# Kernel optimization log

Hardware: AMD Instinct MI355X
Metric: run time of the kernel (lower is better)

The kernel has to match this reference:

```python
import jax, jax.numpy as jnp
import numpy as np
from functools import partial

T, B, V, E, H = 512, 64, 256, 256, 512  # seq, batch, vocab, embed, lstm_hidden


def _lstm_dir(x_proj, W_hh, h0, c0):
    # x_proj: [T, B, 4H] (input projection + bias precomputed); scan only the recurrent matmul
    def step(carry, xp):
        h, c = carry
        gates = xp + h @ W_hh.T                       # [B, 4H]
        i, f, g, o = jnp.split(gates, 4, axis=-1)     # PyTorch gate order i,f,g,o
        i = jax.nn.sigmoid(i); f = jax.nn.sigmoid(f)
        g = jnp.tanh(g); o = jax.nn.sigmoid(o)
        c = f * c + i * g
        h = o * jnp.tanh(c)
        return (h, c), h
    _, hs = jax.lax.scan(step, (h0, c0), x_proj)
    return hs  # [T, B, H]


def setup_inputs() -> dict:
    key = jax.random.key(0)
    ks = jax.random.split(key, 10)
    u = lambda k, shape, s: jax.random.uniform(k, shape, jnp.float32, -s, s)
    bound = 1.0 / np.sqrt(H)
    return {
        "tokens": jax.random.randint(ks[0], (T, B), 0, V, dtype=jnp.int32),
        "h0": jnp.zeros((2, B, H), jnp.float32),
        "c0": jnp.zeros((2, B, H), jnp.float32),
        "embed_table": jax.random.normal(ks[1], (V, E), jnp.float32),
        "W_ih_f": u(ks[2], (4 * H, E), bound),
        "W_hh_f": u(ks[3], (4 * H, H), bound),
        "b_f": u(ks[4], (4 * H,), bound),   # b_ih + b_hh fused
        "W_ih_b": u(ks[5], (4 * H, E), bound),
        "W_hh_b": u(ks[6], (4 * H, H), bound),
        "b_b": u(ks[7], (4 * H,), bound),
        "W_W": u(ks[8], (2 * H, 2 * H), 0.1),
        "b_att": jnp.zeros((2 * H,), jnp.float32),  # bias_char [2H,1] squeezed; uninit in torch
        "w_proj": u(ks[9], (2 * H,), 0.1),           # weight_proj_char [2H,1] squeezed
    }


def reference(tokens, h0, c0, embed_table, W_ih_f, W_hh_f, b_f,
              W_ih_b, W_hh_b, b_b, W_W, b_att, w_proj):
    embedded = embed_table[tokens]                           # [T, B, E]
    # forward direction
    xp_f = jnp.einsum('tbe,ge->tbg', embedded, W_ih_f) + b_f
    out_f = _lstm_dir(xp_f, W_hh_f, h0[0], c0[0])            # [T, B, H]
    # backward direction (reverse time)
    xp_b = jnp.einsum('tbe,ge->tbg', embedded[::-1], W_ih_b) + b_b
    out_b = _lstm_dir(xp_b, W_hh_b, h0[1], c0[1])[::-1]      # [T, B, H]
    output = jnp.concatenate([out_f, out_b], axis=-1)        # [T, B, 2H]
    # additive attention: tanh(out @ W_W + b) . w_proj, softmax over T
    squish = jnp.tanh(jnp.einsum('tbh,hk->tbk', output, W_W) + b_att)
    scores = jnp.einsum('tbk,k->tb', squish, w_proj)         # [T, B]
    attn = jax.nn.softmax(scores, axis=0)                    # softmax over time
    char_vectors = jnp.einsum('tb,tbh->bh', attn, output)    # [B, 2H]
    return char_vectors
```

## Files before the change

kernel.cpp:

```cpp
#include <hip/hip_runtime.h>

#define T_   512
#define B_   64
#define V_   256
#define E_   256
#define H_   512
#define NWGD 32
#define THR  256

typedef _Float16 f16;
typedef _Float16 f16x8 __attribute__((ext_vector_type(8)));
typedef _Float16 f16x4 __attribute__((ext_vector_type(4)));
typedef float    f32x4 __attribute__((ext_vector_type(4)));

#define WS_CTL      0
#define WS_CTL_END  8192
#define WS_SCORES   WS_CTL_END
#define WS_ATTN     (WS_SCORES + 512*64*4)
#define WS_ZERO_END (WS_ATTN + 512*64*4)
#define WS_TAB      WS_ZERO_END
#define WS_WARR     (WS_TAB + 256*256*2)
#define WS_WWT      (WS_WARR + 2*2048*768*2)
#define WS_HBUF     (WS_WWT + 1024*1024*2)
#define WS_OUT      (WS_HBUF + 2*2*64*512*2)
#define WS_END      (WS_OUT + (size_t)512*64*1024*2)

__device__ inline int load_int_sc1(const int* p) {
    int v;
    asm volatile("global_load_dword %0, %1, off sc1\n\ts_waitcnt vmcnt(0)"
                 : "=v"(v) : "v"(p) : "memory");
    return v;
}

__device__ inline void store_int_sc1(int* p, int v) {
    asm volatile("global_store_dword %0, %1, off sc1"
                 :: "v"(p), "v"(v) : "memory");
}

__device__ inline void store_f16_sc1(f16* p, float x) {
    f16 h = (f16)x;
    unsigned int w = (unsigned int)__builtin_bit_cast(unsigned short, h);
    asm volatile("global_store_short %0, %1, off sc1"
                 :: "v"(p), "v"(w) : "memory");
}

__device__ inline void load8_sc1(const f16* p,
    f16x8& r0, f16x8& r1, f16x8& r2, f16x8& r3,
    f16x8& r4, f16x8& r5, f16x8& r6, f16x8& r7) {
    asm volatile(
        "global_load_dwordx4 %0, %8, off sc1\n\t"
        "global_load_dwordx4 %1, %8, off offset:16 sc1\n\t"
        "global_load_dwordx4 %2, %8, off offset:32 sc1\n\t"
        "global_load_dwordx4 %3, %8, off offset:48 sc1\n\t"
        "global_load_dwordx4 %4, %8, off offset:64 sc1\n\t"
        "global_load_dwordx4 %5, %8, off offset:80 sc1\n\t"
        "global_load_dwordx4 %6, %8, off offset:96 sc1\n\t"
        "global_load_dwordx4 %7, %8, off offset:112 sc1\n\t"
        "s_waitcnt vmcnt(0)"
        : "=&v"(r0), "=&v"(r1), "=&v"(r2), "=&v"(r3),
          "=&v"(r4), "=&v"(r5), "=&v"(r6), "=&v"(r7)
        : "v"(p) : "memory");
}

__device__ inline void drain_vm() {
    asm volatile("s_waitcnt vmcnt(0)" ::: "memory");
}

__global__ void k_setup_table(const float* __restrict__ et, f16* __restrict__ tab) {
    int i = blockIdx.x * 256 + threadIdx.x;
    tab[i] = (f16)et[i];
}

__global__ void k_setup_wwt(const float* __restrict__ ww, f16* __restrict__ wwt) {
    int i = blockIdx.x * 256 + threadIdx.x;
    int col = i >> 10, h = i & 1023;
    wwt[(col << 10) + h] = (f16)ww[(h << 10) + col];
}

__global__ void k_setup_warr(const float* __restrict__ wihf, const float* __restrict__ whhf,
                             const float* __restrict__ wihb, const float* __restrict__ whhb,
                             f16* __restrict__ warr) {
    int i = blockIdx.x * 256 + threadIdx.x;
    int k = i % 768;
    int r = i / 768;
    int colp = r & 63;
    int wg   = (r >> 6) & 31;
    int dir  = r >> 11;
    int gate = colp >> 4, u = colp & 15;
    int row = gate * 512 + wg * 16 + u;
    const float* wih = dir ? wihb : wihf;
    const float* whh = dir ? whhb : whhf;
    float v = (k < 256) ? wih[row * 256 + k] : whh[row * 512 + (k - 256)];
    warr[i] = (f16)v;
}

#define A_ROWB  1536
#define LDS_A_BYTES   (64 * A_ROWB)
#define LDS_G_BYTES   (64 * 65 * 4)
#define LDS_C_BYTES   (64 * 16 * 4)
#define LDS_TOTAL     (LDS_A_BYTES + LDS_G_BYTES + LDS_C_BYTES)

__device__ inline int swz(int row, int byteInRow) {
    return byteInRow ^ ((((byteInRow >> 8) + 5 * row) & 7) << 4);
}

__launch_bounds__(THR, 1)
__global__ void k_lstm(const int* __restrict__ tokens,
                       const float* __restrict__ h0, const float* __restrict__ c0,
                       const float* __restrict__ b_f, const float* __restrict__ b_b,
                       const f16* __restrict__ tab, const f16* __restrict__ warr,
                       f16* __restrict__ hbuf, f16* __restrict__ outcat,
                       int* __restrict__ ctl) {
    extern __shared__ __align__(16) char smem[];
    char*  A    = smem;
    float* gate = (float*)(smem + LDS_A_BYTES);
    float* cst  = (float*)(smem + LDS_A_BYTES + LDS_G_BYTES);

    const int tid = threadIdx.x;
    const int dir = blockIdx.x >> 5, wg = blockIdx.x & 31;

    int* flags = ctl + 64 + dir * 512;

    const int l = tid & 63, w = tid >> 6;
    const int mh = w >> 1, nh = w & 1;

    f16x8 bf[2][24];
#pragma unroll
    for (int n = 0; n < 2; ++n) {
#pragma unroll
        for (int kt = 0; kt < 24; ++kt) {
            int colp = nh * 32 + n * 16 + (l & 15);
            long off = ((long)((dir * 32 + wg) * 64 + colp)) * 768 + kt * 32 + (l >> 4) * 8;
            bf[n][kt] = *(const f16x8*)(warr + off);
        }
    }
    const float* bv = dir ? b_b : b_f;
    const int u_t = tid & 15;
    float bias[4];
#pragma unroll
    for (int g = 0; g < 4; ++g) bias[g] = bv[g * 512 + wg * 16 + u_t];

#pragma unroll
    for (int r = 0; r < 4; ++r) {
        int p = r * 256 + tid;
        int b = p >> 4, u = p & 15;
        int ug = wg * 16 + u;
        cst[b * 16 + u] = c0[(dir * 64 + b) * 512 + ug];
        store_f16_sc1(hbuf + ((0 * 2 + dir) * 64 + b) * 512 + ug,
                      h0[(dir * 64 + b) * 512 + ug]);
    }
    drain_vm();
    __syncthreads();
    if (tid == 0) store_int_sc1(flags + wg * 16, 1);

    const int row_t = tid >> 2, part = tid & 3;

#pragma unroll 1
    for (int s = 0; s < 512; ++s) {
        const int t_act = dir ? (511 - s) : s;

        {
            int tok = tokens[t_act * 64 + row_t];
            const f16* src = tab + tok * 256 + part * 64;
            char* base = A + row_t * A_ROWB;
            f16x8 e[8];
#pragma unroll
            for (int c = 0; c < 8; ++c) e[c] = *(const f16x8*)(src + c * 8);
#pragma unroll
            for (int c = 0; c < 8; ++c)
                *(f16x8*)(base + swz(row_t, part * 128 + c * 16)) = e[c];
        }

        {
            const int* fp = flags + (l & 31) * 16;
            const int target = s + 1;
            int guard = 0;
            while (true) {
                int v = load_int_sc1(fp);
                if (__all(v >= target)) break;
                if (++guard > 32768) break;
            }
        }

        {
            const f16* src = hbuf + (((s & 1) * 2 + dir) * 64 + row_t) * 512 + part * 128;
            char* base = A + row_t * A_ROWB;
            f16x8 r0, r1, r2, r3, r4, r5, r6, r7;
            load8_sc1(src, r0, r1, r2, r3, r4, r5, r6, r7);
            *(f16x8*)(base + swz(row_t, 512 + part * 256 +   0)) = r0;
            *(f16x8*)(base + swz(row_t, 512 + part * 256 +  16)) = r1;
            *(f16x8*)(base + swz(row_t, 512 + part * 256 +  32)) = r2;
            *(f16x8*)(base + swz(row_t, 512 + part * 256 +  48)) = r3;
            *(f16x8*)(base + swz(row_t, 512 + part * 256 +  64)) = r4;
            *(f16x8*)(base + swz(row_t, 512 + part * 256 +  80)) = r5;
            *(f16x8*)(base + swz(row_t, 512 + part * 256 +  96)) = r6;
            *(f16x8*)(base + swz(row_t, 512 + part * 256 + 112)) = r7;
            load8_sc1(src + 64, r0, r1, r2, r3, r4, r5, r6, r7);
            *(f16x8*)(base + swz(row_t, 512 + part * 256 + 128)) = r0;
            *(f16x8*)(base + swz(row_t, 512 + part * 256 + 144)) = r1;
            *(f16x8*)(base + swz(row_t, 512 + part * 256 + 160)) = r2;
            *(f16x8*)(base + swz(row_t, 512 + part * 256 + 176)) = r3;
            *(f16x8*)(base + swz(row_t, 512 + part * 256 + 192)) = r4;
            *(f16x8*)(base + swz(row_t, 512 + part * 256 + 208)) = r5;
            *(f16x8*)(base + swz(row_t, 512 + part * 256 + 224)) = r6;
            *(f16x8*)(base + swz(row_t, 512 + part * 256 + 240)) = r7;
        }
        __syncthreads();

        f32x4 acc[2][2];
#pragma unroll
        for (int m = 0; m < 2; ++m)
#pragma unroll
            for (int n = 0; n < 2; ++n)
                acc[m][n] = (f32x4){0.f, 0.f, 0.f, 0.f};
        const int arow0 = mh * 32 + (l & 15);
        const int koffB = (l >> 4) * 16;
#pragma unroll
        for (int kt = 0; kt < 24; ++kt) {
            int binr = kt * 64 + koffB;
            f16x8 a0 = *(const f16x8*)(A + arow0 * A_ROWB + swz(arow0, binr));
            f16x8 a1 = *(const f16x8*)(A + (arow0 + 16) * A_ROWB + swz(arow0 + 16, binr));
            acc[0][0] = __builtin_amdgcn_mfma_f32_16x16x32_f16(a0, bf[0][kt], acc[0][0], 0, 0, 0);
            acc[0][1] = __builtin_amdgcn_mfma_f32_16x16x32_f16(a0, bf[1][kt], acc[0][1], 0, 0, 0);
            acc[1][0] = __builtin_amdgcn_mfma_f32_16x16x32_f16(a1, bf[0][kt], acc[1][0], 0, 0, 0);
            acc[1][1] = __builtin_amdgcn_mfma_f32_16x16x32_f16(a1, bf[1][kt], acc[1][1], 0, 0, 0);
        }
#pragma unroll
        for (int m = 0; m < 2; ++m)
#pragma unroll
            for (int n = 0; n < 2; ++n)
#pragma unroll
                for (int q = 0; q < 4; ++q) {
                    int brow = mh * 32 + m * 16 + (l >> 4) * 4 + q;
                    int col  = nh * 32 + n * 16 + (l & 15);
                    gate[brow * 65 + col] = acc[m][n][q];
                }
        __syncthreads();

#pragma unroll
        for (int r = 0; r < 4; ++r) {
            int p = r * 256 + tid;
            int b = p >> 4, u = p & 15;
            float gi = gate[b * 65 +  0 + u] + bias[0];
            float gf = gate[b * 65 + 16 + u] + bias[1];
            float gg = gate[b * 65 + 32 + u] + bias[2];
            float go = gate[b * 65 + 48 + u] + bias[3];
            float si = 1.f / (1.f + __expf(-gi));
            float sf = 1.f / (1.f + __expf(-gf));
            float tg = tanhf(gg);
            float so = 1.f / (1.f + __expf(-go));
            float c = sf * cst[b * 16 + u] + si * tg;
            float h = so * tanhf(c);
            cst[b * 16 + u] = c;
            int ug = wg * 16 + u;
            store_f16_sc1(hbuf + ((((s + 1) & 1) * 2 + dir) * 64 + b) * 512 + ug, h);
            outcat[((long)t_act * 64 + b) * 1024 + dir * 512 + ug] = (f16)h;
        }
        drain_vm();
        __syncthreads();
        if (tid == 0) store_int_sc1(flags + wg * 16, s + 2);
    }
}

__global__ void k_attn_gemm(const f16* __restrict__ outcat, const f16* __restrict__ wwt,
                            const float* __restrict__ b_att, const float* __restrict__ w_proj,
                            float* __restrict__ scores) {
    __shared__ __align__(16) f16 A2[64][136];
    __shared__ __align__(16) f16 B2[64][136];
    __shared__ float sq[64][68];
    const int tid = threadIdx.x;
    const int mb = blockIdx.x >> 4, nb = blockIdx.x & 15;
    const int r0 = mb * 64, c0 = nb * 64;
    const int l = tid & 63, w = tid >> 6;
    const int mh = w >> 1, nhf = w & 1;

    f32x4 acc[2][2];
#pragma unroll
    for (int m = 0; m < 2; ++m)
#pragma unroll
        for (int n = 0; n < 2; ++n)
            acc[m][n] = (f32x4){0.f, 0.f, 0.f, 0.f};

    for (int kc = 0; kc < 8; ++kc) {
        int k0 = kc * 128;
        {
            int row = tid >> 2, seg = tid & 3;
            const f16* sa = outcat + (long)(r0 + row) * 1024 + k0 + seg * 32;
            const f16* sb = wwt + (long)(c0 + row) * 1024 + k0 + seg * 32;
#pragma unroll
            for (int j = 0; j < 4; ++j) {
                *(f16x8*)(&A2[row][seg * 32 + j * 8]) = *(const f16x8*)(sa + j * 8);
                *(f16x8*)(&B2[row][seg * 32 + j * 8]) = *(const f16x8*)(sb + j * 8);
            }
        }
        __syncthreads();
        const int kofs = (l >> 4) * 8;
#pragma unroll
        for (int kt = 0; kt < 4; ++kt) {
            int ko = kt * 32 + kofs;
            f16x8 a0 = *(const f16x8*)(&A2[mh * 32 + (l & 15)][ko]);
            f16x8 a1 = *(const f16x8*)(&A2[mh * 32 + 16 + (l & 15)][ko]);
            f16x8 b0 = *(const f16x8*)(&B2[nhf * 32 + (l & 15)][ko]);
            f16x8 b1 = *(const f16x8*)(&B2[nhf * 32 + 16 + (l & 15)][ko]);
            acc[0][0] = __builtin_amdgcn_mfma_f32_16x16x32_f16(a0, b0, acc[0][0], 0, 0, 0);
            acc[0][1] = __builtin_amdgcn_mfma_f32_16x16x32_f16(a0, b1, acc[0][1], 0, 0, 0);
            acc[1][0] = __builtin_amdgcn_mfma_f32_16x16x32_f16(a1, b0, acc[1][0], 0, 0, 0);
            acc[1][1] = __builtin_amdgcn_mfma_f32_16x16x32_f16(a1, b1, acc[1][1], 0, 0, 0);
        }
        __syncthreads();
    }
#pragma unroll
    for (int m = 0; m < 2; ++m)
#pragma unroll
        for (int n = 0; n < 2; ++n)
#pragma unroll
            for (int q = 0; q < 4; ++q) {
                int rl = mh * 32 + m * 16 + (l >> 4) * 4 + q;
                int cl = nhf * 32 + n * 16 + (l & 15);
                int cg = c0 + cl;
                sq[rl][cl] = tanhf(acc[m][n][q] + b_att[cg]) * w_proj[cg];
            }
    __syncthreads();
    if (tid < 64) {
        float s = 0.f;
#pragma unroll
        for (int c2 = 0; c2 < 64; ++c2) s += sq[tid][c2];
        atomicAdd(scores + r0 + tid, s);
    }
}

__global__ void k_softmax(const float* __restrict__ scores, float* __restrict__ attn) {
    const int b = blockIdx.x, tid = threadIdx.x;
    __shared__ float redm[4];
    __shared__ float reds[4];
    float v0 = scores[(tid * 2 + 0) * 64 + b];
    float v1 = scores[(tid * 2 + 1) * 64 + b];
    float m = fmaxf(v0, v1);
#pragma unroll
    for (int off = 32; off; off >>= 1) m = fmaxf(m, __shfl_down(m, off));
    if ((tid & 63) == 0) redm[tid >> 6] = m;
    __syncthreads();
    m = fmaxf(fmaxf(redm[0], redm[1]), fmaxf(redm[2], redm[3]));
    float e0 = __expf(v0 - m), e1 = __expf(v1 - m);
    float s = e0 + e1;
#pragma unroll
    for (int off = 32; off; off >>= 1) s += __shfl_down(s, off);
    if ((tid & 63) == 0) reds[tid >> 6] = s;
    __syncthreads();
    s = (reds[0] + reds[1]) + (reds[2] + reds[3]);
    float inv = 1.f / s;
    attn[(tid * 2 + 0) * 64 + b] = e0 * inv;
    attn[(tid * 2 + 1) * 64 + b] = e1 * inv;
}

__global__ void k_wsum(const float* __restrict__ attn, const f16* __restrict__ outcat,
                       float* __restrict__ out) {
    const int b = blockIdx.x, tid = threadIdx.x;
    float a0 = 0.f, a1 = 0.f, a2 = 0.f, a3 = 0.f;
    for (int t = 0; t < 512; ++t) {
        float at = attn[t * 64 + b];
        f16x4 v = *(const f16x4*)(outcat + ((long)t * 64 + b) * 1024 + tid * 4);
        a0 += at * (float)v[0];
        a1 += at * (float)v[1];
        a2 += at * (float)v[2];
        a3 += at * (float)v[3];
    }
    float* dst = out + b * 1024 + tid * 4;
    dst[0] = a0; dst[1] = a1; dst[2] = a2; dst[3] = a3;
}

extern "C" void kernel_launch(void* const* d_in, const int* in_sizes, int n_in,
                              void* d_out, int out_size, void* d_ws, size_t ws_size,
                              hipStream_t stream) {
    if (ws_size < WS_END) return;

    const int*   tokens = (const int*)d_in[0];
    const float* h0     = (const float*)d_in[1];
    const float* c0     = (const float*)d_in[2];
    const float* etab   = (const float*)d_in[3];
    const float* wihf   = (const float*)d_in[4];
    const float* whhf   = (const float*)d_in[5];
    const float* b_f    = (const float*)d_in[6];
    const float* wihb   = (const float*)d_in[7];
    const float* whhb   = (const float*)d_in[8];
    const float* b_b    = (const float*)d_in[9];
    const float* ww     = (const float*)d_in[10];
    const float* b_att  = (const float*)d_in[11];
    const float* w_proj = (const float*)d_in[12];
    float* out = (float*)d_out;

    char* ws = (char*)d_ws;
    int*   ctl    = (int*)(ws + WS_CTL);
    float* scores = (float*)(ws + WS_SCORES);
    float* attn   = (float*)(ws + WS_ATTN);
    f16*   tab    = (f16*)(ws + WS_TAB);
    f16*   warr   = (f16*)(ws + WS_WARR);
    f16*   wwt    = (f16*)(ws + WS_WWT);
    f16*   hbuf   = (f16*)(ws + WS_HBUF);
    f16*   outcat = (f16*)(ws + WS_OUT);

    hipMemsetAsync(d_ws, 0, WS_ZERO_END, stream);

    k_setup_table<<<256, 256, 0, stream>>>(etab, tab);
    k_setup_wwt<<<4096, 256, 0, stream>>>(ww, wwt);
    k_setup_warr<<<12288, 256, 0, stream>>>(wihf, whhf, wihb, whhb, warr);

    static int lds_set = 0;
    if (!lds_set) {
        hipFuncSetAttribute((const void*)k_lstm,
                            hipFuncAttributeMaxDynamicSharedMemorySize, LDS_TOTAL);
        lds_set = 1;
    }
    k_lstm<<<64, THR, LDS_TOTAL, stream>>>(tokens, h0, c0, b_f, b_b,
                                           tab, warr, hbuf, outcat, ctl);

    k_attn_gemm<<<8192, 256, 0, stream>>>(outcat, wwt, b_att, w_proj, scores);
    k_softmax<<<64, 256, 0, stream>>>(scores, attn);
    k_wsum<<<64, 256, 0, stream>>>(attn, outcat, out);
}
```

Before: 4.088 ms.

## Load LSTM MFMA A-operands directly from global into registers, bypassing LDS staging

The recurrent step no longer stages the embedding row and previous hidden state into a swizzled LDS tile before the MFMA loop. Each lane now loads its MFMA A fragments straight from global memory into registers. The hidden-state loads are split into two halves with partial vmcnt waits so MFMAs overlap the remaining loads, and next-step tokens are prefetched. The gate epilogue is vectorised to four units per thread with 64-bit h stores. This removes one barrier and the LDS write/read round trip per step. In exchange it costs more VGPRs and issues redundant global loads, because wave pairs with nh=0 and nh=1 fetch the same rows. The spin-wait guard is also lowered.

```diff
diff --git a/kernel.cpp b/kernel.cpp
--- a/kernel.cpp
+++ b/kernel.cpp
@@ -37,34 +37,24 @@
                  :: "v"(p), "v"(v) : "memory");
 }
 
-__device__ inline void store_f16_sc1(f16* p, float x) {
-    f16 h = (f16)x;
-    unsigned int w = (unsigned int)__builtin_bit_cast(unsigned short, h);
-    asm volatile("global_store_short %0, %1, off sc1"
-                 :: "v"(p), "v"(w) : "memory");
-}
-
-__device__ inline void load8_sc1(const f16* p,
-    f16x8& r0, f16x8& r1, f16x8& r2, f16x8& r3,
-    f16x8& r4, f16x8& r5, f16x8& r6, f16x8& r7) {
-    asm volatile(
-        "global_load_dwordx4 %0, %8, off sc1\n\t"
-        "global_load_dwordx4 %1, %8, off offset:16 sc1\n\t"
-        "global_load_dwordx4 %2, %8, off offset:32 sc1\n\t"
-        "global_load_dwordx4 %3, %8, off offset:48 sc1\n\t"
-        "global_load_dwordx4 %4, %8, off offset:64 sc1\n\t"
-        "global_load_dwordx4 %5, %8, off offset:80 sc1\n\t"
-        "global_load_dwordx4 %6, %8, off offset:96 sc1\n\t"
-        "global_load_dwordx4 %7, %8, off offset:112 sc1\n\t"
-        "s_waitcnt vmcnt(0)"
-        : "=&v"(r0), "=&v"(r1), "=&v"(r2), "=&v"(r3),
-          "=&v"(r4), "=&v"(r5), "=&v"(r6), "=&v"(r7)
-        : "v"(p) : "memory");
+__device__ inline void store_f16x4_sc1(f16* p, f16x4 v) {
+    asm volatile("global_store_dwordx2 %0, %1, off sc1"
+                 :: "v"(p), "v"(v) : "memory");
 }
 
 __device__ inline void drain_vm() {
     asm volatile("s_waitcnt vmcnt(0)" ::: "memory");
 }
+
+#define LD4(dst, base, OFFB) \
+    asm volatile("global_load_dwordx4 %0, %1, off offset:" #OFFB \
+                 : "=v"(dst) : "v"(base))
+#define LD4S(dst, base, OFFB) \
+    asm volatile("global_load_dwordx4 %0, %1, off offset:" #OFFB " sc1" \
+                 : "=v"(dst) : "v"(base))
+#define WAITVM(N) do { \
+    asm volatile("s_waitcnt vmcnt(" #N ")" ::: "memory"); \
+    __builtin_amdgcn_sched_barrier(0); } while (0)
 
 __global__ void k_setup_table(const float* __restrict__ et, f16* __restrict__ tab) {
     int i = blockIdx.x * 256 + threadIdx.x;
@@ -94,15 +84,7 @@
     warr[i] = (f16)v;
 }
 
-#define A_ROWB  1536
-#define LDS_A_BYTES   (64 * A_ROWB)
-#define LDS_G_BYTES   (64 * 65 * 4)
-#define LDS_C_BYTES   (64 * 16 * 4)
-#define LDS_TOTAL     (LDS_A_BYTES + LDS_G_BYTES + LDS_C_BYTES)
-
-__device__ inline int swz(int row, int byteInRow) {
-    return byteInRow ^ ((((byteInRow >> 8) + 5 * row) & 7) << 4);
-}
+#define GSTR 68
 
 __launch_bounds__(THR, 1)
 __global__ void k_lstm(const int* __restrict__ tokens,
@@ -111,64 +93,68 @@
                        const f16* __restrict__ tab, const f16* __restrict__ warr,
                        f16* __restrict__ hbuf, f16* __restrict__ outcat,
                        int* __restrict__ ctl) {
-    extern __shared__ __align__(16) char smem[];
-    char*  A    = smem;
-    float* gate = (float*)(smem + LDS_A_BYTES);
-    float* cst  = (float*)(smem + LDS_A_BYTES + LDS_G_BYTES);
+    __shared__ float gate[64 * GSTR];
+    __shared__ float cst[64 * 16];
 
     const int tid = threadIdx.x;
     const int dir = blockIdx.x >> 5, wg = blockIdx.x & 31;
-
     int* flags = ctl + 64 + dir * 512;
 
     const int l = tid & 63, w = tid >> 6;
     const int mh = w >> 1, nh = w & 1;
-
-    f16x8 bf[2][24];
-#pragma unroll
-    for (int n = 0; n < 2; ++n) {
-#pragma unroll
-        for (int kt = 0; kt < 24; ++kt) {
-            int colp = nh * 32 + n * 16 + (l & 15);
-            long off = ((long)((dir * 32 + wg) * 64 + colp)) * 768 + kt * 32 + (l >> 4) * 8;
-            bf[n][kt] = *(const f16x8*)(warr + off);
-        }
-    }
+    const int r0 = mh * 32 + (l & 15), r1 = r0 + 16;
+    const int kofs = (l >> 4) * 8;
+
+    f16x8 bf0[24], bf1[24];
+#pragma unroll
+    for (int kt = 0; kt < 24; ++kt) {
+        int colp0 = nh * 32 + 0 * 16 + (l & 15);
+        int colp1 = nh * 32 + 1 * 16 + (l & 15);
+        long base = (long)((dir * 32 + wg) * 64) * 768;
+        bf0[kt] = *(const f16x8*)(warr + base + (long)colp0 * 768 + kt * 32 + kofs);
+        bf1[kt] = *(const f16x8*)(warr + base + (long)colp1 * 768 + kt * 32 + kofs);
+    }
+
+    const int pb = tid >> 2;
+    const int u0 = (tid & 3) * 4;
     const float* bv = dir ? b_b : b_f;
-    const int u_t = tid & 15;
-    float bias[4];
-#pragma unroll
-    for (int g = 0; g < 4; ++g) bias[g] = bv[g * 512 + wg * 16 + u_t];
-
-#pragma unroll
-    for (int r = 0; r < 4; ++r) {
-        int p = r * 256 + tid;
-        int b = p >> 4, u = p & 15;
-        int ug = wg * 16 + u;
-        cst[b * 16 + u] = c0[(dir * 64 + b) * 512 + ug];
-        store_f16_sc1(hbuf + ((0 * 2 + dir) * 64 + b) * 512 + ug,
-                      h0[(dir * 64 + b) * 512 + ug]);
+    f32x4 bias[4];
+#pragma unroll
+    for (int g = 0; g < 4; ++g)
+        bias[g] = *(const f32x4*)(bv + g * 512 + wg * 16 + u0);
+
+    {
+        f32x4 cv = *(const f32x4*)(c0 + (dir * 64 + pb) * 512 + wg * 16 + u0);
+        *(f32x4*)(cst + pb * 16 + u0) = cv;
+        f32x4 h4 = *(const f32x4*)(h0 + (dir * 64 + pb) * 512 + wg * 16 + u0);
+        f16x4 hv;
+#pragma unroll
+        for (int j = 0; j < 4; ++j) hv[j] = (f16)h4[j];
+        store_f16x4_sc1(hbuf + ((0 * 2 + dir) * 64 + pb) * 512 + wg * 16 + u0, hv);
     }
     drain_vm();
     __syncthreads();
     if (tid == 0) store_int_sc1(flags + wg * 16, 1);
 
-    const int row_t = tid >> 2, part = tid & 3;
+    int tok0 = tokens[(dir ? 511 : 0) * 64 + r0];
+    int tok1 = tokens[(dir ? 511 : 0) * 64 + r1];
 
 #pragma unroll 1
     for (int s = 0; s < 512; ++s) {
         const int t_act = dir ? (511 - s) : s;
 
+        f16x8 e0[8], e1[8];
         {
-            int tok = tokens[t_act * 64 + row_t];
-            const f16* src = tab + tok * 256 + part * 64;
-            char* base = A + row_t * A_ROWB;
-            f16x8 e[8];
-#pragma unroll
-            for (int c = 0; c < 8; ++c) e[c] = *(const f16x8*)(src + c * 8);
-#pragma unroll
-            for (int c = 0; c < 8; ++c)
-                *(f16x8*)(base + swz(row_t, part * 128 + c * 16)) = e[c];
+            const f16* p0 = tab + tok0 * 256 + kofs;
+            const f16* p1 = tab + tok1 * 256 + kofs;
+            LD4(e0[0], p0, 0);   LD4(e1[0], p1, 0);
+            LD4(e0[1], p0, 64);  LD4(e1[1], p1, 64);
+            LD4(e0[2], p0, 128); LD4(e1[2], p1, 128);
+            LD4(e0[3], p0, 192); LD4(e1[3], p1, 192);
+            LD4(e0[4], p0, 256); LD4(e1[4], p1, 256);
+            LD4(e0[5], p0, 320); LD4(e1[5], p1, 320);
+            LD4(e0[6], p0, 384); LD4(e1[6], p1, 384);
+            LD4(e0[7], p0, 448); LD4(e1[7], p1, 448);
         }
 
         {
@@ -178,83 +164,103 @@
             while (true) {
                 int v = load_int_sc1(fp);
                 if (__all(v >= target)) break;
-                if (++guard > 32768) break;
+                if (++guard > 8192) break;
             }
         }
+        __builtin_amdgcn_sched_barrier(0);
+
+        const f16* hbase = hbuf + (long)(((s & 1) * 2 + dir) * 64) * 512;
+        const f16* pr0 = hbase + r0 * 512 + kofs;
+        const f16* pr1 = hbase + r1 * 512 + kofs;
+        f16x8 ha0[8], ha1[8], hc0[8], hc1[8];
+        LD4S(ha0[0], pr0, 0);   LD4S(ha1[0], pr1, 0);
+        LD4S(ha0[1], pr0, 64);  LD4S(ha1[1], pr1, 64);
+        LD4S(ha0[2], pr0, 128); LD4S(ha1[2], pr1, 128);
+        LD4S(ha0[3], pr0, 192); LD4S(ha1[3], pr1, 192);
+        LD4S(ha0[4], pr0, 256); LD4S(ha1[4], pr1, 256);
+        LD4S(ha0[5], pr0, 320); LD4S(ha1[5], pr1, 320);
+        LD4S(ha0[6], pr0, 384); LD4S(ha1[6], pr1, 384);
+        LD4S(ha0[7], pr0, 448); LD4S(ha1[7], pr1, 448);
+
+        f32x4 a00 = {0.f,0.f,0.f,0.f}, a01 = {0.f,0.f,0.f,0.f};
+        f32x4 a10 = {0.f,0.f,0.f,0.f}, a11 = {0.f,0.f,0.f,0.f};
+#pragma unroll
+        for (int kt = 0; kt < 8; ++kt) {
+            a00 = __builtin_amdgcn_mfma_f32_16x16x32_f16(e0[kt], bf0[kt], a00, 0, 0, 0);
+            a01 = __builtin_amdgcn_mfma_f32_16x16x32_f16(e0[kt], bf1[kt], a01, 0, 0, 0);
+            a10 = __builtin_amdgcn_mfma_f32_16x16x32_f16(e1[kt], bf0[kt], a10, 0, 0, 0);
+            a11 = __builtin_amdgcn_mfma_f32_16x16x32_f16(e1[kt], bf1[kt], a11, 0, 0, 0);
+        }
+
+        LD4S(hc0[0], pr0, 512); LD4S(hc1[0], pr1, 512);
+        LD4S(hc0[1], pr0, 576); LD4S(hc1[1], pr1, 576);
+        LD4S(hc0[2], pr0, 640); LD4S(hc1[2], pr1, 640);
+        LD4S(hc0[3], pr0, 704); LD4S(hc1[3], pr1, 704);
+        LD4S(hc0[4], pr0, 768); LD4S(hc1[4], pr1, 768);
+        LD4S(hc0[5], pr0, 832); LD4S(hc1[5], pr1, 832);
+        LD4S(hc0[6], pr0, 896); LD4S(hc1[6], pr1, 896);
+        LD4S(hc0[7], pr0, 960); LD4S(hc1[7], pr1, 960);
+
+        WAITVM(16);
+#pragma unroll
+        for (int kt = 0; kt < 8; ++kt) {
+            a00 = __builtin_amdgcn_mfma_f32_16x16x32_f16(ha0[kt], bf0[kt + 8], a00, 0, 0, 0);
+            a01 = __builtin_amdgcn_mfma_f32_16x16x32_f16(ha0[kt], bf1[kt + 8], a01, 0, 0, 0);
+            a10 = __builtin_amdgcn_mfma_f32_16x16x32_f16(ha1[kt], bf0[kt + 8], a10, 0, 0, 0);
+            a11 = __builtin_amdgcn_mfma_f32_16x16x32_f16(ha1[kt], bf1[kt + 8], a11, 0, 0, 0);
+        }
+        WAITVM(0);
+#pragma unroll
+        for (int kt = 0; kt < 8; ++kt) {
+            a00 = __builtin_amdgcn_mfma_f32_16x16x32_f16(hc0[kt], bf0[kt + 16], a00, 0, 0, 0);
+            a01 = __builtin_amdgcn_mfma_f32_16x16x32_f16(hc0[kt], bf1[kt + 16], a01, 0, 0, 0);
+            a10 = __builtin_amdgcn_mfma_f32_16x16x32_f16(hc1[kt], bf0[kt + 16], a10, 0, 0, 0);
+            a11 = __builtin_amdgcn_mfma_f32_16x16x32_f16(hc1[kt], bf1[kt + 16], a11, 0, 0, 0);
+        }
+
+#pragma unroll
+        for (int q = 0; q < 4; ++q) {
+            int br0 = mh * 32 + (l >> 4) * 4 + q;
+            int br1 = br0 + 16;
+            int cl0 = nh * 32 + (l & 15);
+            gate[br0 * GSTR + cl0]      = a00[q];
+            gate[br0 * GSTR + cl0 + 16] = a01[q];
+            gate[br1 * GSTR + cl0]      = a10[q];
+            gate[br1 * GSTR + cl0 + 16] = a11[q];
+        }
+        __syncthreads();
 
         {
-            const f16* src = hbuf + (((s & 1) * 2 + dir) * 64 + row_t) * 512 + part * 128;
-            char* base = A + row_t * A_ROWB;
-            f16x8 r0, r1, r2, r3, r4, r5, r6, r7;
-            load8_sc1(src, r0, r1, r2, r3, r4, r5, r6, r7);
-            *(f16x8*)(base + swz(row_t, 512 + part * 256 +   0)) = r0;
-            *(f16x8*)(base + swz(row_t, 512 + part * 256 +  16)) = r1;
-            *(f16x8*)(base + swz(row_t, 512 + part * 256 +  32)) = r2;
-            *(f16x8*)(base + swz(row_t, 512 + part * 256 +  48)) = r3;
-            *(f16x8*)(base + swz(row_t, 512 + part * 256 +  64)) = r4;
-            *(f16x8*)(base + swz(row_t, 512 + part * 256 +  80)) = r5;
-            *(f16x8*)(base + swz(row_t, 512 + part * 256 +  96)) = r6;
-            *(f16x8*)(base + swz(row_t, 512 + part * 256 + 112)) = r7;
-            load8_sc1(src + 64, r0, r1, r2, r3, r4, r5, r6, r7);
-            *(f16x8*)(base + swz(row_t, 512 + part * 256 + 128)) = r0;
-            *(f16x8*)(base + swz(row_t, 512 + part * 256 + 144)) = r1;
-            *(f16x8*)(base + swz(row_t, 512 + part * 256 + 160)) = r2;
-            *(f16x8*)(base + swz(row_t, 512 + part * 256 + 176)) = r3;
-            *(f16x8*)(base + swz(row_t, 512 + part * 256 + 192)) = r4;
-            *(f16x8*)(base + swz(row_t, 512 + part * 256 + 208)) = r5;
-            *(f16x8*)(base + swz(row_t, 512 + part * 256 + 224)) = r6;
-            *(f16x8*)(base + swz(row_t, 512 + part * 256 + 240)) = r7;
-        }
-        __syncthreads();
-
-        f32x4 acc[2][2];
-#pragma unroll
-        for (int m = 0; m < 2; ++m)
-#pragma unroll
-            for (int n = 0; n < 2; ++n)
-                acc[m][n] = (f32x4){0.f, 0.f, 0.f, 0.f};
-        const int arow0 = mh * 32 + (l & 15);
-        const int koffB = (l >> 4) * 16;
-#pragma unroll
-        for (int kt = 0; kt < 24; ++kt) {
-            int binr = kt * 64 + koffB;
-            f16x8 a0 = *(const f16x8*)(A + arow0 * A_ROWB + swz(arow0, binr));
-            f16x8 a1 = *(const f16x8*)(A + (arow0 + 16) * A_ROWB + swz(arow0 + 16, binr));
-            acc[0][0] = __builtin_amdgcn_mfma_f32_16x16x32_f16(a0, bf[0][kt], acc[0][0], 0, 0, 0);
-            acc[0][1] = __builtin_amdgcn_mfma_f32_16x16x32_f16(a0, bf[1][kt], acc[0][1], 0, 0, 0);
-            acc[1][0] = __builtin_amdgcn_mfma_f32_16x16x32_f16(a1, bf[0][kt], acc[1][0], 0, 0, 0);
-            acc[1][1] = __builtin_amdgcn_mfma_f32_16x16x32_f16(a1, bf[1][kt], acc[1][1], 0, 0, 0);
-        }
-#pragma unroll
-        for (int m = 0; m < 2; ++m)
-#pragma unroll
-            for (int n = 0; n < 2; ++n)
-#pragma unroll
-                for (int q = 0; q < 4; ++q) {
-                    int brow = mh * 32 + m * 16 + (l >> 4) * 4 + q;
-                    int col  = nh * 32 + n * 16 + (l & 15);
-                    gate[brow * 65 + col] = acc[m][n][q];
-                }
-        __syncthreads();
-
-#pragma unroll
-        for (int r = 0; r < 4; ++r) {
-            int p = r * 256 + tid;
-            int b = p >> 4, u = p & 15;
-            float gi = gate[b * 65 +  0 + u] + bias[0];
-            float gf = gate[b * 65 + 16 + u] + bias[1];
-            float gg = gate[b * 65 + 32 + u] + bias[2];
-            float go = gate[b * 65 + 48 + u] + bias[3];
-            float si = 1.f / (1.f + __expf(-gi));
-            float sf = 1.f / (1.f + __expf(-gf));
-            float tg = tanhf(gg);
-            float so = 1.f / (1.f + __expf(-go));
-            float c = sf * cst[b * 16 + u] + si * tg;
-            float h = so * tanhf(c);
-            cst[b * 16 + u] = c;
-            int ug = wg * 16 + u;
-            store_f16_sc1(hbuf + ((((s + 1) & 1) * 2 + dir) * 64 + b) * 512 + ug, h);
-            outcat[((long)t_act * 64 + b) * 1024 + dir * 512 + ug] = (f16)h;
+            int sn = (s < 511) ? (s + 1) : 511;
+            int tn = dir ? (511 - sn) : sn;
+            tok0 = tokens[tn * 64 + r0];
+            tok1 = tokens[tn * 64 + r1];
+        }
+        {
+            f32x4 g0 = *(const f32x4*)(gate + pb * GSTR +  0 + u0);
+            f32x4 g1 = *(const f32x4*)(gate + pb * GSTR + 16 + u0);
+            f32x4 g2 = *(const f32x4*)(gate + pb * GSTR + 32 + u0);
+            f32x4 g3 = *(const f32x4*)(gate + pb * GSTR + 48 + u0);
+            f32x4 cv = *(const f32x4*)(cst + pb * 16 + u0);
+            f16x4 hv;
+#pragma unroll
+            for (int j = 0; j < 4; ++j) {
+                float gi = g0[j] + bias[0][j];
+                float gf = g1[j] + bias[1][j];
+                float gg = g2[j] + bias[2][j];
+                float go = g3[j] + bias[3][j];
+                float si = 1.f / (1.f + __expf(-gi));
+                float sf = 1.f / (1.f + __expf(-gf));
+                float tg = tanhf(gg);
+                float so = 1.f / (1.f + __expf(-go));
+                float c = sf * cv[j] + si * tg;
+                float h = so * tanhf(c);
+                cv[j] = c;
+                hv[j] = (f16)h;
+            }
+            *(f32x4*)(cst + pb * 16 + u0) = cv;
+            store_f16x4_sc1(hbuf + ((((s + 1) & 1) * 2 + dir) * 64 + pb) * 512 + wg * 16 + u0, hv);
+            *(f16x4*)(outcat + ((long)t_act * 64 + pb) * 1024 + dir * 512 + wg * 16 + u0) = hv;
         }
         drain_vm();
         __syncthreads();
@@ -405,14 +411,8 @@
     k_setup_wwt<<<4096, 256, 0, stream>>>(ww, wwt);
     k_setup_warr<<<12288, 256, 0, stream>>>(wihf, whhf, wihb, whhb, warr);
 
-    static int lds_set = 0;
-    if (!lds_set) {
-        hipFuncSetAttribute((const void*)k_lstm,
-                            hipFuncAttributeMaxDynamicSharedMemorySize, LDS_TOTAL);
-        lds_set = 1;
-    }
-    k_lstm<<<64, THR, LDS_TOTAL, stream>>>(tokens, h0, c0, b_f, b_b,
-                                           tab, warr, hbuf, outcat, ctl);
+    k_lstm<<<64, THR, 0, stream>>>(tokens, h0, c0, b_f, b_b,
+                                   tab, warr, hbuf, outcat, ctl);
 
     k_attn_gemm<<<8192, 256, 0, stream>>>(outcat, wwt, b_att, w_proj, scores);
     k_softmax<<<64, 256, 0, stream>>>(scores, attn);
```

After: 4.376 ms. 1.07x slower.
